# Kernel tuning notes

Hardware: AMD Instinct MI355X
Metric: run time of the kernel (lower is better)

Reference implementation:

```python
import jax, jax.numpy as jnp
import numpy as np

N_CAPS, R, CIN, COUT = 10, 1152, 8, 16  # digit caps, primary caps (32*6*6), caps dims
B = 256


def setup_inputs() -> dict:
    key = jax.random.key(0)
    k1, k2 = jax.random.split(key)
    x = jax.random.normal(k1, (B, R, CIN), dtype=jnp.float32)
    # learned transform W: [num_capsules, num_route_nodes, in_channels, out_channels]
    W = jax.random.normal(k2, (N_CAPS, R, CIN, COUT), dtype=jnp.float32)
    return {"x": x, "W": W}


def squash(t, axis=-1):
    sq = jnp.sum(t * t, axis=axis, keepdims=True)
    return sq / (1.0 + sq) * t / jnp.sqrt(sq)


def reference(x, W):
    # u_hat = (x[None,:,:,None,:] @ W[:,None]) -> [N_CAPS, B, R, 1, COUT]; squeeze the 1.
    u_hat = jnp.einsum('bri,nrio->nbro', x, W)  # [N, B, R, O]
    # NOTE: the original forward returns v_j INSIDE the routing loop, so exactly one
    # iteration executes: b_ij = 0 => c_ij = softmax(zeros, dim=route) = 1/R (uniform).
    c = 1.0 / u_hat.shape[2]
    s = jnp.sum(c * u_hat, axis=2, keepdims=True)  # [N, B, 1, O]
    v = squash(s, axis=-1)
    return v[:, :, :, None, :]  # [N, B, 1, 1, O] to match torch v_j shape
```

## Files before the change

kernel.cpp:

```cpp
#include <hip/hip_runtime.h>

#define RNODES 1152
#define KDIM 9216
#define COUT 16
#define NCAPS 10
#define WSTRIDE (KDIM*COUT)

#define LROW 40
#define WBUF (NCAPS*COUT*LROW)
#define STEPS 9
#define SPLITS 32
#define NBLK 256
#define PARTL (32*COUT*NCAPS)
#define PARTL4 (PARTL/4)

using bf16x8 = __attribute__((ext_vector_type(8))) short;
using f32x4  = __attribute__((ext_vector_type(4))) float;

__device__ __forceinline__ unsigned short f2bf(float f) {
  unsigned int u = __builtin_bit_cast(unsigned int, f);
  return (unsigned short)((u + 0x8000u) >> 16);
}

__global__ __launch_bounds__(256, 1) void caps_gemm(const float* __restrict__ x,
                                                    const float* __restrict__ W,
                                                    float* __restrict__ ws) {
  __shared__ unsigned short wbuf[2][WBUF];
  const int tid = threadIdx.x;
  const int bid = blockIdx.x;
  const int mt  = bid >> 5;
  const int ks  = bid & 31;
  const int b0  = mt * 32;
  const int k0  = ks * (STEPS * 32);

  const int lane = tid & 63;
  const int wv   = tid >> 6;
  const int p    = wv >> 1;
  const int h    = wv & 1;
  const int q    = lane >> 4;
  const int m16  = lane & 15;

  const int c4 = tid >> 5;
  const int kl = tid & 31;

  const float* xrow = x + (size_t)(b0 + p * 16 + m16) * KDIM + k0 + q * 8;

  float4 pw[3][5];
  float4 pa[3][2];

  auto load_step = [&](int s, int slot) {
#pragma unroll
    for (int j = 0; j < 5; ++j) {
      const int cc = c4 + 8 * j;
      const int n  = cc >> 2, o4 = (cc & 3) << 2;
      pw[slot][j] = *(const float4*)(W + (size_t)n * WSTRIDE +
                                     (size_t)(k0 + s * 32 + kl) * COUT + o4);
    }
    pa[slot][0] = *(const float4*)(xrow + s * 32);
    pa[slot][1] = *(const float4*)(xrow + s * 32 + 4);
  };

  load_step(0, 0);
  load_step(1, 1);
  load_step(2, 2);

  f32x4 acc[5];
#pragma unroll
  for (int i = 0; i < 5; ++i) acc[i] = (f32x4){0.f, 0.f, 0.f, 0.f};

#pragma unroll
  for (int s = 0; s < STEPS; ++s) {
    const int slot = s % 3;
    unsigned short* b = &wbuf[s & 1][0];
#pragma unroll
    for (int j = 0; j < 5; ++j) {
      const int cc = c4 + 8 * j;
      const int cb = cc * 4 * LROW + kl;
      b[cb + 0 * LROW] = f2bf(pw[slot][j].x);
      b[cb + 1 * LROW] = f2bf(pw[slot][j].y);
      b[cb + 2 * LROW] = f2bf(pw[slot][j].z);
      b[cb + 3 * LROW] = f2bf(pw[slot][j].w);
    }
    __syncthreads();

    bf16x8 a;
    a[0] = (short)f2bf(pa[slot][0].x); a[1] = (short)f2bf(pa[slot][0].y);
    a[2] = (short)f2bf(pa[slot][0].z); a[3] = (short)f2bf(pa[slot][0].w);
    a[4] = (short)f2bf(pa[slot][1].x); a[5] = (short)f2bf(pa[slot][1].y);
    a[6] = (short)f2bf(pa[slot][1].z); a[7] = (short)f2bf(pa[slot][1].w);

    if (s + 3 < STEPS) load_step(s + 3, slot);

#pragma unroll
    for (int j = 0; j < 5; ++j) {
      const int nt = h * 5 + j;
      bf16x8 bf = *(const bf16x8*)&b[(nt * COUT + m16) * LROW + q * 8];
      acc[j] = __builtin_amdgcn_mfma_f32_16x16x32_bf16(a, bf, acc[j], 0, 0, 0);
    }
  }

  float* P = ws + (size_t)bid * PARTL;
  const int prow = p * 16 + q * 4;
#pragma unroll
  for (int j = 0; j < 5; ++j)
#pragma unroll
    for (int r = 0; r < 4; ++r)
      P[(h * 5 + j) * 512 + (prow + r) * COUT + m16] = acc[j][r];
}

__global__ __launch_bounds__(128, 1) void caps_reduce(const float* __restrict__ ws,
                                                      float* __restrict__ out) {
  const int f  = blockIdx.x * 128 + threadIdx.x;
  const int n  = f >> 10;
  const int b  = (f >> 2) & 255;
  const int o4 = f & 3;
  const int mt = b >> 5, row = b & 31;

  const float4* base = (const float4*)ws + (size_t)(mt * SPLITS) * PARTL4
                       + n * 128 + row * 4 + o4;
  float4 s0 = {0,0,0,0}, s1 = {0,0,0,0}, s2 = {0,0,0,0}, s3 = {0,0,0,0};
#pragma unroll
  for (int kk = 0; kk < SPLITS; kk += 4) {
    float4 a0 = base[(size_t)(kk + 0) * PARTL4];
    float4 a1 = base[(size_t)(kk + 1) * PARTL4];
    float4 a2 = base[(size_t)(kk + 2) * PARTL4];
    float4 a3 = base[(size_t)(kk + 3) * PARTL4];
    s0.x += a0.x; s0.y += a0.y; s0.z += a0.z; s0.w += a0.w;
    s1.x += a1.x; s1.y += a1.y; s1.z += a1.z; s1.w += a1.w;
    s2.x += a2.x; s2.y += a2.y; s2.z += a2.z; s2.w += a2.w;
    s3.x += a3.x; s3.y += a3.y; s3.z += a3.z; s3.w += a3.w;
  }
  const float inv = 1.0f / (float)RNODES;
  float4 s;
  s.x = ((s0.x + s1.x) + (s2.x + s3.x)) * inv;
  s.y = ((s0.y + s1.y) + (s2.y + s3.y)) * inv;
  s.z = ((s0.z + s1.z) + (s2.z + s3.z)) * inv;
  s.w = ((s0.w + s1.w) + (s2.w + s3.w)) * inv;

  float sq = s.x * s.x + s.y * s.y + s.z * s.z + s.w * s.w;
  sq += __shfl_xor(sq, 1);
  sq += __shfl_xor(sq, 2);
  const float g = sqrtf(sq) / (1.0f + sq);
  s.x *= g; s.y *= g; s.z *= g; s.w *= g;

  ((float4*)out)[f] = s;
}

extern "C" void kernel_launch(void* const* d_in, const int* in_sizes, int n_in,
                              void* d_out, int out_size, void* d_ws, size_t ws_size,
                              hipStream_t stream) {
  const float* x = (const float*)d_in[0];
  const float* W = (const float*)d_in[1];
  float* ws  = (float*)d_ws;
  float* out = (float*)d_out;

  caps_gemm<<<dim3(NBLK), dim3(256), 0, stream>>>(x, W, ws);
  caps_reduce<<<dim3(80), dim3(128), 0, stream>>>(ws, out);
}
```

Measured before the change: 71.39 us.

## Retile capsule GEMM to 16-row M tiles with 16 K-splits and packed bf16 stores

```diff
diff --git a/kernel.cpp b/kernel.cpp
--- a/kernel.cpp
+++ b/kernel.cpp
@@ -8,15 +8,21 @@
 
 #define LROW 40
 #define WBUF (NCAPS*COUT*LROW)
-#define STEPS 9
-#define SPLITS 32
+#define DSTEPS 9
+#define SPLITS 16
+#define MTILES 16
 #define NBLK 256
-#define PARTL (32*COUT*NCAPS)
+#define PARTL (MTILES*COUT*NCAPS)
 #define PARTL4 (PARTL/4)
 
 using bf16x8 = __attribute__((ext_vector_type(8))) short;
 using f32x4  = __attribute__((ext_vector_type(4))) float;
 
+__device__ __forceinline__ unsigned int pack2(float lo, float hi) {
+  unsigned int a = __builtin_bit_cast(unsigned int, lo);
+  unsigned int b = __builtin_bit_cast(unsigned int, hi);
+  return ((a + 0x8000u) >> 16) | ((b + 0x8000u) & 0xFFFF0000u);
+}
 __device__ __forceinline__ unsigned short f2bf(float f) {
   unsigned int u = __builtin_bit_cast(unsigned int, f);
   return (unsigned short)((u + 0x8000u) >> 16);
@@ -25,99 +31,120 @@
 __global__ __launch_bounds__(256, 1) void caps_gemm(const float* __restrict__ x,
                                                     const float* __restrict__ W,
                                                     float* __restrict__ ws) {
-  __shared__ unsigned short wbuf[2][WBUF];
+  __shared__ unsigned short wbuf[4][WBUF];
   const int tid = threadIdx.x;
   const int bid = blockIdx.x;
-  const int mt  = bid >> 5;
-  const int ks  = bid & 31;
-  const int b0  = mt * 32;
-  const int k0  = ks * (STEPS * 32);
+  const int mt  = bid >> 4;
+  const int ks  = bid & 15;
+  const int b0  = mt * MTILES;
+  const int k0  = ks * (DSTEPS * 64);
 
   const int lane = tid & 63;
   const int wv   = tid >> 6;
-  const int p    = wv >> 1;
-  const int h    = wv & 1;
   const int q    = lane >> 4;
   const int m16  = lane & 15;
 
-  const int c4 = tid >> 5;
-  const int kl = tid & 31;
+  const int ncap = (wv < 2) ? 3 : 2;
+  const int cap0 = (wv < 2) ? wv * 3 : 6 + (wv - 2) * 2;
 
-  const float* xrow = x + (size_t)(b0 + p * 16 + m16) * KDIM + k0 + q * 8;
+  int u_cc[5], u_kp[5], u_sub[5];
+#pragma unroll
+  for (int j = 0; j < 5; ++j) {
+    const int u = j * 256 + tid;
+    u_kp[j]  = u & 15;
+    u_cc[j]  = (u >> 4) % 40;
+    u_sub[j] = u / 640;
+  }
 
-  float4 pw[3][5];
-  float4 pa[3][2];
+  const float* xrow = x + (size_t)(b0 + m16) * KDIM + k0 + q * 8;
 
-  auto load_step = [&](int s, int slot) {
+  float4 pw[2][5][2];
+  float4 xa[2][2][2];
+
+  auto load_w = [&](int ds, int slot) {
 #pragma unroll
     for (int j = 0; j < 5; ++j) {
-      const int cc = c4 + 8 * j;
-      const int n  = cc >> 2, o4 = (cc & 3) << 2;
-      pw[slot][j] = *(const float4*)(W + (size_t)n * WSTRIDE +
-                                     (size_t)(k0 + s * 32 + kl) * COUT + o4);
+      const int n  = u_cc[j] >> 2, o4 = (u_cc[j] & 3) << 2;
+      const float* base = W + (size_t)n * WSTRIDE +
+                          (size_t)(k0 + ds * 64 + u_sub[j] * 32 + 2 * u_kp[j]) * COUT + o4;
+      pw[slot][j][0] = *(const float4*)(base);
+      pw[slot][j][1] = *(const float4*)(base + COUT);
     }
-    pa[slot][0] = *(const float4*)(xrow + s * 32);
-    pa[slot][1] = *(const float4*)(xrow + s * 32 + 4);
+  };
+  auto load_x = [&](int ds, int slot) {
+#pragma unroll
+    for (int sub = 0; sub < 2; ++sub) {
+      xa[slot][sub][0] = *(const float4*)(xrow + ds * 64 + sub * 32);
+      xa[slot][sub][1] = *(const float4*)(xrow + ds * 64 + sub * 32 + 4);
+    }
   };
 
-  load_step(0, 0);
-  load_step(1, 1);
-  load_step(2, 2);
+  load_w(0, 0);
+  load_w(1, 1);
+  load_x(0, 0);
 
-  f32x4 acc[5];
+  f32x4 acc[3];
 #pragma unroll
-  for (int i = 0; i < 5; ++i) acc[i] = (f32x4){0.f, 0.f, 0.f, 0.f};
+  for (int i = 0; i < 3; ++i) acc[i] = (f32x4){0.f, 0.f, 0.f, 0.f};
 
-#pragma unroll
-  for (int s = 0; s < STEPS; ++s) {
-    const int slot = s % 3;
-    unsigned short* b = &wbuf[s & 1][0];
+  for (int ds = 0; ds < DSTEPS; ++ds) {
+    const int par = ds & 1;
 #pragma unroll
     for (int j = 0; j < 5; ++j) {
-      const int cc = c4 + 8 * j;
-      const int cb = cc * 4 * LROW + kl;
-      b[cb + 0 * LROW] = f2bf(pw[slot][j].x);
-      b[cb + 1 * LROW] = f2bf(pw[slot][j].y);
-      b[cb + 2 * LROW] = f2bf(pw[slot][j].z);
-      b[cb + 3 * LROW] = f2bf(pw[slot][j].w);
+      const int n  = u_cc[j] >> 2, o4 = (u_cc[j] & 3) << 2;
+      unsigned int* b32 =
+          (unsigned int*)&wbuf[par * 2 + u_sub[j]][(n * COUT + o4) * LROW + 2 * u_kp[j]];
+      const int lr2 = LROW / 2;
+#pragma unroll
+      for (int r = 0; r < 4; ++r)
+        b32[r * lr2] = pack2(pw[par][j][0][r], pw[par][j][1][r]);
     }
     __syncthreads();
 
-    bf16x8 a;
-    a[0] = (short)f2bf(pa[slot][0].x); a[1] = (short)f2bf(pa[slot][0].y);
-    a[2] = (short)f2bf(pa[slot][0].z); a[3] = (short)f2bf(pa[slot][0].w);
-    a[4] = (short)f2bf(pa[slot][1].x); a[5] = (short)f2bf(pa[slot][1].y);
-    a[6] = (short)f2bf(pa[slot][1].z); a[7] = (short)f2bf(pa[slot][1].w);
-
-    if (s + 3 < STEPS) load_step(s + 3, slot);
+    if (ds + 2 < DSTEPS) load_w(ds + 2, par);
+    if (ds + 1 < DSTEPS) load_x(ds + 1, (ds + 1) & 1);
 
 #pragma unroll
-    for (int j = 0; j < 5; ++j) {
-      const int nt = h * 5 + j;
-      bf16x8 bf = *(const bf16x8*)&b[(nt * COUT + m16) * LROW + q * 8];
-      acc[j] = __builtin_amdgcn_mfma_f32_16x16x32_bf16(a, bf, acc[j], 0, 0, 0);
+    for (int sub = 0; sub < 2; ++sub) {
+      const unsigned short* b = &wbuf[par * 2 + sub][0];
+      uint4 av;
+      av.x = pack2(xa[par][sub][0].x, xa[par][sub][0].y);
+      av.y = pack2(xa[par][sub][0].z, xa[par][sub][0].w);
+      av.z = pack2(xa[par][sub][1].x, xa[par][sub][1].y);
+      av.w = pack2(xa[par][sub][1].z, xa[par][sub][1].w);
+      const bf16x8 a = __builtin_bit_cast(bf16x8, av);
+#pragma unroll
+      for (int j = 0; j < 3; ++j) {
+        if (j < ncap) {
+          const int nt = cap0 + j;
+          bf16x8 bf = *(const bf16x8*)&b[(nt * COUT + m16) * LROW + q * 8];
+          acc[j] = __builtin_amdgcn_mfma_f32_16x16x32_bf16(a, bf, acc[j], 0, 0, 0);
+        }
+      }
     }
   }
 
   float* P = ws + (size_t)bid * PARTL;
-  const int prow = p * 16 + q * 4;
 #pragma unroll
-  for (int j = 0; j < 5; ++j)
+  for (int j = 0; j < 3; ++j) {
+    if (j < ncap) {
 #pragma unroll
-    for (int r = 0; r < 4; ++r)
-      P[(h * 5 + j) * 512 + (prow + r) * COUT + m16] = acc[j][r];
+      for (int r = 0; r < 4; ++r)
+        P[(cap0 + j) * 256 + (q * 4 + r) * COUT + m16] = acc[j][r];
+    }
+  }
 }
 
-__global__ __launch_bounds__(128, 1) void caps_reduce(const float* __restrict__ ws,
-                                                      float* __restrict__ out) {
-  const int f  = blockIdx.x * 128 + threadIdx.x;
+__global__ __launch_bounds__(64, 1) void caps_reduce(const float* __restrict__ ws,
+                                                     float* __restrict__ out) {
+  const int f  = blockIdx.x * 64 + threadIdx.x;
   const int n  = f >> 10;
   const int b  = (f >> 2) & 255;
   const int o4 = f & 3;
-  const int mt = b >> 5, row = b & 31;
+  const int mt = b >> 4, row = b & 15;
 
   const float4* base = (const float4*)ws + (size_t)(mt * SPLITS) * PARTL4
-                       + n * 128 + row * 4 + o4;
+                       + n * 64 + row * 4 + o4;
   float4 s0 = {0,0,0,0}, s1 = {0,0,0,0}, s2 = {0,0,0,0}, s3 = {0,0,0,0};
 #pragma unroll
   for (int kk = 0; kk < SPLITS; kk += 4) {
@@ -155,5 +182,5 @@
   float* out = (float*)d_out;
 
   caps_gemm<<<dim3(NBLK), dim3(256), 0, stream>>>(x, W, ws);
-  caps_reduce<<<dim3(80), dim3(128), 0, stream>>>(ws, out);
+  caps_reduce<<<dim3(160), dim3(64), 0, stream>>>(ws, out);
 }
```

After: 78.66 us. 10.2% more time.
